# Performance work log

Measured on AMD Instinct MI355X. Metric: run time of the kernel, lower is better.

The kernel has to match this reference:

```python
import jax, jax.numpy as jnp
import numpy as np

N_NODES = 100000
NUM_ETYPE = 4
HEADS = 4
HID = 32
IN_CH = 128
EDGE_CH = 32
N_EDGES = 800000
BATCH = 1024
NEG = 5


def setup_inputs() -> dict:
    key = jax.random.key(0)
    ks = jax.random.split(key, 24)

    def w(k, shape, s=0.05):
        return jax.random.normal(k, shape, dtype=jnp.float32) * s

    inp = {}
    inp["edge_index"] = jax.random.randint(ks[0], (2, N_EDGES), 0, N_NODES)
    inp["edge_type"] = jax.random.randint(ks[1], (N_EDGES,), 0, NUM_ETYPE)
    inp["n_id"] = jax.random.randint(ks[2], (BATCH * (2 + NEG),), 0, N_NODES)
    inp["neg_sample_num"] = NEG
    inp["id_emb"] = w(ks[3], (N_NODES, IN_CH), 0.1)
    dims = [IN_CH, HEADS * HID]
    for i in range(2):
        d_in = dims[i]
        base = 4 + i * 7
        inp[f"W{i}"] = w(ks[base], (d_in, HEADS * HID))
        inp[f"Wres{i}"] = w(ks[base + 1], (d_in, HEADS * HID))
        inp[f"al{i}"] = w(ks[base + 2], (HEADS, HID))
        inp[f"ar{i}"] = w(ks[base + 3], (HEADS, HID))
        inp[f"ae{i}"] = w(ks[base + 4], (HEADS, EDGE_CH))
        inp[f"eemb{i}"] = w(ks[base + 5], (NUM_ETYPE, EDGE_CH))
        inp[f"We{i}"] = w(ks[base + 6], (EDGE_CH, HEADS * EDGE_CH))
    inp["pW1"] = w(ks[18], (2 * HEADS * HID, HID))
    inp["pb1"] = jnp.zeros((HID,), jnp.float32)
    inp["pW2"] = w(ks[19], (HID, 1))
    inp["pb2"] = jnp.zeros((1,), jnp.float32)
    return inp


def _leaky(x):
    return jnp.where(x > 0, x, 0.2 * x)  # LeakyReLU(0.2)


def _conv(h, src, dst, etype, W, Wres, al, ar, ae, eemb, We):
    """Simple-HGN style edge-typed graph attention conv with linear residual."""
    n = h.shape[0]
    feat = (h @ W).reshape(n, HEADS, HID)                      # [N,H,D]
    ef = (eemb @ We).reshape(NUM_ETYPE, HEADS, EDGE_CH)        # [T,H,De]
    el = jnp.einsum('nhd,hd->nh', feat, al)                    # [N,H]
    er = jnp.einsum('nhd,hd->nh', feat, ar)                    # [N,H]
    ee = jnp.einsum('thd,hd->th', ef, ae)                      # [T,H]
    logits = _leaky(el[src] + er[dst] + ee[etype])             # [E,H]
    # numerically stable per-destination softmax over incoming edges
    m = jax.ops.segment_max(logits, dst, num_segments=n)
    m = jnp.where(jnp.isfinite(m), m, jnp.zeros_like(m))
    a = jnp.exp(logits - m[dst])
    denom = jax.ops.segment_sum(a, dst, num_segments=n)
    alpha = a / (denom[dst] + 1e-16)                           # [E,H]
    out = jax.ops.segment_sum(feat[src] * alpha[:, :, None], dst, num_segments=n)
    return out.reshape(n, HEADS * HID) + h @ Wres


def reference(edge_index, edge_type, n_id, neg_sample_num, id_emb,
              W0, Wres0, al0, ar0, ae0, eemb0, We0,
              W1, Wres1, al1, ar1, ae1, eemb1, We1,
              pW1, pb1, pW2, pb2):
    src, dst = edge_index[0], edge_index[1]
    x = _conv(id_emb, src, dst, edge_type, W0, Wres0, al0, ar0, ae0, eemb0, We0)
    x = jax.nn.relu(x)  # relu between layers; dropout inactive at eval
    x = _conv(x, src, dst, edge_type, W1, Wres1, al1, ar1, ae1, eemb1, We1)
    b = n_id.shape[0] // (2 + neg_sample_num)
    out = x[n_id[:b]]
    pos = x[n_id[b:2 * b]]
    neg = x[n_id[2 * b:]]
    tiled = jnp.repeat(out, neg_sample_num, axis=0)  # repeat(1,neg).reshape(-1,D)

    def head(z):
        return _leaky(z @ pW1 + pb1) @ pW2 + pb2

    pos_logit = head(jnp.concatenate([out, pos], axis=-1))
    neg_logits = head(jnp.concatenate([tiled, neg], axis=-1))
    return pos_logit, neg_logits
```

## Files before the change

kernel.cpp:

```cpp
#include <hip/hip_runtime.h>
#include <hip/hip_bf16.h>
#include <math.h>

#define HEADS 4
#define HID 32
#define DIM 128
#define NEGS 5

typedef short s16x8 __attribute__((ext_vector_type(8)));
typedef short s16x4 __attribute__((ext_vector_type(4)));
typedef unsigned short u16x8 __attribute__((ext_vector_type(8)));
typedef float f32x4 __attribute__((ext_vector_type(4)));

__device__ __forceinline__ unsigned short f2bf_rn(float x) {
    unsigned int u = __float_as_uint(x);
    unsigned int r = (u + 0x7FFFu + ((u >> 16) & 1u)) >> 16;
    return (unsigned short)r;
}
__device__ __forceinline__ float bf2f(unsigned short b) {
    return __uint_as_float(((unsigned int)b) << 16);
}

__global__ void k_setup(const float* __restrict__ W0, const float* __restrict__ Wres0,
                        const float* __restrict__ W1, const float* __restrict__ Wres1,
                        const float* __restrict__ eemb0, const float* __restrict__ We0,
                        const float* __restrict__ ae0,
                        const float* __restrict__ eemb1, const float* __restrict__ We1,
                        const float* __restrict__ ae1,
                        unsigned short* __restrict__ bt, float* __restrict__ eeB,
                        int* __restrict__ zbase, int zn) {
    int idx = blockIdx.x * 256 + threadIdx.x;

    for (int i = idx; i < zn; i += 65536) zbase[i] = 0;

    {
        int layer = idx >> 15;
        int r = idx & 32767;
        int k = r >> 8;
        int n = r & 255;
        const float* src = layer ? ((n < 128) ? W1 : Wres1) : ((n < 128) ? W0 : Wres0);
        float x = src[k * 128 + (n & 127)];
        unsigned short h = f2bf_rn(x);
        unsigned short l = f2bf_rn(x - bf2f(h));
        unsigned short* base = bt + (size_t)layer * 2 * 32768;
        base[n * 128 + k] = h;
        base[32768 + n * 128 + k] = l;
    }

    if (idx < 32) {
        int layer = idx >> 4, t = idx & 15;
        const float* eemb = layer ? eemb1 : eemb0;
        const float* We   = layer ? We1 : We0;
        const float* ae   = layer ? ae1 : ae0;
        int et = t >> 2, h = t & 3;
        float s = 0.f;
        for (int d = 0; d < 32; ++d) {
            float ef = 0.f;
            for (int k = 0; k < 32; ++k) ef += eemb[et * 32 + k] * We[k * DIM + h * 32 + d];
            s += ef * ae[h * 32 + d];
        }
        eeB[layer * 16 + t] = s;
    }
}

__global__ void k_flag2(const int* __restrict__ n_id, int* __restrict__ flag2,
                        int* __restrict__ flag1, int M) {
    int i = blockIdx.x * 256 + threadIdx.x;
    if (i < M) { int n = n_id[i]; flag2[n] = 1; flag1[n] = 1; }
}

__global__ void k_histflag(const int* __restrict__ src, const int* __restrict__ dst,
                           const int* __restrict__ flag2,
                           int* __restrict__ counts, int* __restrict__ flag1, int E) {
    int e = blockIdx.x * 256 + threadIdx.x;
    if (e < E) {
        int d = dst[e];
        atomicAdd(&counts[d], 1);
        if (flag2[d]) flag1[src[e]] = 1;
    }
}

__global__ __launch_bounds__(1024) void k_scanA(const int* __restrict__ counts,
                                                int* __restrict__ rowtmp,
                                                int* __restrict__ bsum, int N) {
    __shared__ int s[1024];
    int i = blockIdx.x * 1024 + threadIdx.x;
    int v = (i < N) ? counts[i] : 0;
    s[threadIdx.x] = v;
    __syncthreads();
    for (int off = 1; off < 1024; off <<= 1) {
        int t = (threadIdx.x >= off) ? s[threadIdx.x - off] : 0;
        __syncthreads();
        s[threadIdx.x] += t;
        __syncthreads();
    }
    if (i < N) rowtmp[i] = s[threadIdx.x];
    if (threadIdx.x == 1023) bsum[blockIdx.x] = s[1023];
}

__global__ __launch_bounds__(256) void k_scanC(const int* __restrict__ rowtmp,
                                               const int* __restrict__ counts,
                                               const int* __restrict__ bsum, int nb,
                                               int* __restrict__ row_start,
                                               int* __restrict__ cursor,
                                               const int* __restrict__ flag1,
                                               const int* __restrict__ flag2,
                                               int* __restrict__ list1,
                                               int* __restrict__ list2,
                                               int* __restrict__ cnt1,
                                               int* __restrict__ cnt2, int N) {
    __shared__ int sex[128];
    int tid = threadIdx.x;
    if (tid < 64) {
        int l = tid;
        int a = (2 * l < nb) ? bsum[2 * l] : 0;
        int b = (2 * l + 1 < nb) ? bsum[2 * l + 1] : 0;
        int s = a + b;
        for (int off = 1; off < 64; off <<= 1) {
            int t = __shfl_up(s, off);
            if (l >= off) s += t;
        }
        int excl = s - (a + b);
        sex[2 * l] = excl;
        sex[2 * l + 1] = excl + a;
    }
    __syncthreads();

    int i = blockIdx.x * 256 + tid;
    int lane = tid & 63;
    if (i < N) {
        int st = rowtmp[i] - counts[i] + sex[i >> 10];
        row_start[i] = st;
        cursor[i] = st;
    }

    unsigned long long lt = (lane == 63) ? ~0ull >> 1 : (1ull << lane) - 1;
    bool a = (i < N) && flag1[i];
    unsigned long long m = __ballot(a);
    int base = 0;
    if (lane == 0 && m) base = atomicAdd(cnt1, __popcll(m));
    base = __shfl(base, 0);
    if (a) list1[base + __popcll(m & lt)] = i;

    bool b = (i < N) && flag2[i];
    m = __ballot(b);
    base = 0;
    if (lane == 0 && m) base = atomicAdd(cnt2, __popcll(m));
    base = __shfl(base, 0);
    if (b) list2[base + __popcll(m & lt)] = i;
}

__global__ void k_scatter(const int* __restrict__ dst, int* __restrict__ cursor,
                          int* __restrict__ csr_edge, int E) {
    int e = blockIdx.x * 256 + threadIdx.x;
    if (e < E) {
        int p = atomicAdd(&cursor[dst[e]], 1);
        csr_edge[p] = e;
    }
}

__global__ __launch_bounds__(256, 4) void k_gemm_fused(const float* __restrict__ A,
                                                       const unsigned short* __restrict__ Bhi,
                                                       const unsigned short* __restrict__ Blo,
                                                       unsigned short* __restrict__ featb,
                                                       float* __restrict__ res,
                                                       const float* __restrict__ al,
                                                       const float* __restrict__ ar,
                                                       float* __restrict__ el,
                                                       float* __restrict__ er,
                                                       const int* __restrict__ rowlist,
                                                       const int* __restrict__ rowcnt,
                                                       const int* __restrict__ resflag,
                                                       int N) {
    int limit = rowcnt ? *rowcnt : N;
    int c = blockIdx.x;
    int m0 = blockIdx.y * 64;
    if (m0 >= limit) return;

    __shared__ unsigned short Bh[8192];
    __shared__ unsigned short Bl[8192];
    int tid = threadIdx.x;
    int lane = tid & 63, w = tid >> 6;
    int wm = (w & 1) * 32, wn = (w >> 1) * 32;
    int lr = lane & 15, g = lane >> 4;

#pragma unroll
    for (int i = 0; i < 4; ++i) {
        int f = tid + i * 256;
        int row = f >> 4, g16 = f & 15;
        int off = (row * 256 + ((g16 * 16) ^ ((row & 7) << 4))) >> 1;
        *(u16x8*)&Bh[off] = *(const u16x8*)(Bhi + (size_t)(c * 64 + row) * DIM + g16 * 8);
        *(u16x8*)&Bl[off] = *(const u16x8*)(Blo + (size_t)(c * 64 + row) * DIM + g16 * 8);
    }

    s16x8 afh[2][4], afl[2][4];
#pragma unroll
    for (int fm = 0; fm < 2; ++fm) {
        int idx = m0 + wm + fm * 16 + lr;
        bool valid = idx < limit;
        int grow = 0;
        if (valid) grow = rowlist ? rowlist[idx] : idx;
        const float* ap = A + (size_t)grow * DIM;
#pragma unroll
        for (int ks = 0; ks < 4; ++ks) {
            float4 p = make_float4(0.f, 0.f, 0.f, 0.f);
            float4 q = make_float4(0.f, 0.f, 0.f, 0.f);
            if (valid) {
                p = *(const float4*)(ap + ks * 32 + g * 4);
                q = *(const float4*)(ap + ks * 32 + 16 + g * 4);
            }
            float vv[8] = {p.x, p.y, p.z, p.w, q.x, q.y, q.z, q.w};
            s16x8 hv, lv;
#pragma unroll
            for (int j = 0; j < 8; ++j) {
                unsigned short hh = f2bf_rn(vv[j]);
                hv[j] = (short)hh;
                lv[j] = (short)f2bf_rn(vv[j] - bf2f(hh));
            }
            afh[fm][ks] = hv;
            afl[fm][ks] = lv;
        }
    }
    __syncthreads();

    f32x4 acc[2][2];
#pragma unroll
    for (int fm = 0; fm < 2; ++fm)
#pragma unroll
        for (int fn = 0; fn < 2; ++fn) acc[fm][fn] = (f32x4){0.f, 0.f, 0.f, 0.f};

#pragma unroll
    for (int ks = 0; ks < 4; ++ks) {
        s16x8 bfh[2], bfl[2];
#pragma unroll
        for (int fn = 0; fn < 2; ++fn) {
            int row = wn + fn * 16 + lr;
            int sw = (row & 7) << 4;
            int o1 = (row * 256 + ((ks * 64 + g * 8) ^ sw)) >> 1;
            int o2 = (row * 256 + ((ks * 64 + 32 + g * 8) ^ sw)) >> 1;
            s16x4 p = *(const s16x4*)&Bh[o1];
            s16x4 q = *(const s16x4*)&Bh[o2];
            bfh[fn] = (s16x8){p[0], p[1], p[2], p[3], q[0], q[1], q[2], q[3]};
            p = *(const s16x4*)&Bl[o1];
            q = *(const s16x4*)&Bl[o2];
            bfl[fn] = (s16x8){p[0], p[1], p[2], p[3], q[0], q[1], q[2], q[3]};
        }
#pragma unroll
        for (int fm = 0; fm < 2; ++fm)
#pragma unroll
            for (int fn = 0; fn < 2; ++fn) {
                acc[fm][fn] = __builtin_amdgcn_mfma_f32_16x16x32_bf16(afh[fm][ks], bfh[fn], acc[fm][fn], 0, 0, 0);
                acc[fm][fn] = __builtin_amdgcn_mfma_f32_16x16x32_bf16(afh[fm][ks], bfl[fn], acc[fm][fn], 0, 0, 0);
                acc[fm][fn] = __builtin_amdgcn_mfma_f32_16x16x32_bf16(afl[fm][ks], bfh[fn], acc[fm][fn], 0, 0, 0);
            }
    }

#pragma unroll
    for (int fm = 0; fm < 2; ++fm)
#pragma unroll
        for (int fn = 0; fn < 2; ++fn) {
            int idx0 = m0 + wm + fm * 16 + g * 4;
            int dc = ((c * 64) & 127) + wn + fn * 16 + lr;
#pragma unroll
            for (int r = 0; r < 4; ++r) {
                int idx = idx0 + r;
                if (idx < limit) {
                    int gr = rowlist ? rowlist[idx] : idx;
                    if (c < 2) {
                        featb[(size_t)gr * DIM + dc] = f2bf_rn(acc[fm][fn][r]);
                    } else if (!resflag || resflag[gr]) {
                        res[(size_t)gr * DIM + dc] = acc[fm][fn][r];
                    }
                }
            }
        }

    if (c < 2) {
        int h = c * 2 + (wn >> 5);
        float a0 = al[h * HID + lr], a1 = al[h * HID + 16 + lr];
        float b0 = ar[h * HID + lr], b1 = ar[h * HID + 16 + lr];
#pragma unroll
        for (int fm = 0; fm < 2; ++fm)
#pragma unroll
            for (int r = 0; r < 4; ++r) {
                float ev = acc[fm][0][r] * a0 + acc[fm][1][r] * a1;
                float rv = acc[fm][0][r] * b0 + acc[fm][1][r] * b1;
#pragma unroll
                for (int off = 1; off < 16; off <<= 1) {
                    ev += __shfl_xor(ev, off);
                    rv += __shfl_xor(rv, off);
                }
                if (lr == 0) {
                    int idx = m0 + wm + fm * 16 + g * 4 + r;
                    if (idx < limit) {
                        int node = rowlist ? rowlist[idx] : idx;
                        el[node * 4 + h] = ev;
                        er[node * 4 + h] = rv;
                    }
                }
            }
    }
}

template <int RELU>
__global__ __launch_bounds__(256) void k_agg(const unsigned short* __restrict__ featb,
                                             const float* __restrict__ el,
                                             const float* __restrict__ er,
                                             const float* __restrict__ eeB,
                                             const int* __restrict__ srcArr,
                                             const int* __restrict__ etArr,
                                             const int* __restrict__ csr_edge,
                                             const int* __restrict__ row_start,
                                             const int* __restrict__ counts,
                                             const int* __restrict__ dlist,
                                             const int* __restrict__ dcnt,
                                             float* __restrict__ out) {
    int wv = threadIdx.x >> 6;
    int lane = threadIdx.x & 63;
    int idx = blockIdx.x * 4 + wv;
    if (idx >= *dcnt) return;
    int node = dlist[idx];

    int beg = row_start[node];
    int deg = counts[node];
    int eh = lane & 3;
    float er_v = er[node * 4 + eh];

    float m = -INFINITY;
    for (int base = 0; base < deg; base += 16) {
        int ei = base + (lane >> 2);
        float lg = -INFINITY;
        if (ei < deg) {
            int e = csr_edge[beg + ei];
            float x = el[srcArr[e] * 4 + eh] + er_v + eeB[etArr[e] * 4 + eh];
            lg = (x > 0.f) ? x : 0.2f * x;
        }
        m = fmaxf(m, lg);
    }
    for (int off = 4; off < 64; off <<= 1) m = fmaxf(m, __shfl_xor(m, off));

    float denom = 0.f, acc0 = 0.f, acc1 = 0.f;
    int h1 = lane >> 5;
    for (int base = 0; base < deg; base += 16) {
        int ei = base + (lane >> 2);
        float wgt = 0.f;
        int s = 0;
        if (ei < deg) {
            int e = csr_edge[beg + ei];
            s = srcArr[e];
            float x = el[s * 4 + eh] + er_v + eeB[etArr[e] * 4 + eh];
            x = (x > 0.f) ? x : 0.2f * x;
            wgt = expf(x - m);
            denom += wgt;
        }
        int cnt = min(16, deg - base);
        for (int j = 0; j < cnt; ++j) {
            int sj = __shfl(s, j * 4);
            float w1 = __shfl(wgt, j * 4 + h1);
            float w2 = __shfl(wgt, j * 4 + 2 + h1);
            acc0 += w1 * bf2f(featb[(size_t)sj * DIM + lane]);
            acc1 += w2 * bf2f(featb[(size_t)sj * DIM + 64 + lane]);
        }
    }
    for (int off = 4; off < 64; off <<= 1) denom += __shfl_xor(denom, off);
    float d1 = __shfl(denom, h1);
    float d2 = __shfl(denom, 2 + h1);

    float r0 = out[(size_t)node * DIM + lane] + acc0 / (d1 + 1e-16f);
    float r1 = out[(size_t)node * DIM + 64 + lane] + acc1 / (d2 + 1e-16f);
    if (RELU) { r0 = fmaxf(r0, 0.f); r1 = fmaxf(r1, 0.f); }
    out[(size_t)node * DIM + lane] = r0;
    out[(size_t)node * DIM + 64 + lane] = r1;
}

__global__ __launch_bounds__(256) void k_head(const float* __restrict__ x1,
                                              const int* __restrict__ n_id,
                                              const float* __restrict__ pW1,
                                              const float* __restrict__ pb1,
                                              const float* __restrict__ pW2,
                                              const float* __restrict__ pb2,
                                              float* __restrict__ dout, int B) {
    int o = blockIdx.x * 4 + (threadIdx.x >> 6);
    int lane = threadIdx.x & 63;
    int total = B + B * NEGS;
    if (o >= total) return;
    int a, c;
    if (o < B) { a = n_id[o]; c = n_id[B + o]; }
    else { int j = o - B; a = n_id[j / NEGS]; c = n_id[2 * B + j]; }

    int j = lane & 31;
    int half = lane >> 5;
    int row = half ? c : a;
    const float* z = x1 + (size_t)row * DIM;
    const float* w = pW1 + (half ? 128 * 32 : 0);
    float t = 0.f;
#pragma unroll 8
    for (int k = 0; k < 128; ++k) t += z[k] * w[k * 32 + j];
    t += __shfl_xor(t, 32);
    t += pb1[j];
    t = (t > 0.f) ? t : 0.2f * t;
    float r = t * pW2[j];
    for (int off = 1; off < 32; off <<= 1) r += __shfl_xor(r, off);
    if (lane == 0) dout[o] = r + pb2[0];
}

extern "C" void kernel_launch(void* const* d_in, const int* in_sizes, int n_in,
                              void* d_out, int out_size, void* d_ws, size_t ws_size,
                              hipStream_t stream) {
    const int* edge_index = (const int*)d_in[0];
    const int* etype      = (const int*)d_in[1];
    const int* n_id       = (const int*)d_in[2];
    const float* id_emb   = (const float*)d_in[4];
    const float* W0    = (const float*)d_in[5];
    const float* Wres0 = (const float*)d_in[6];
    const float* al0   = (const float*)d_in[7];
    const float* ar0   = (const float*)d_in[8];
    const float* ae0   = (const float*)d_in[9];
    const float* eemb0 = (const float*)d_in[10];
    const float* We0   = (const float*)d_in[11];
    const float* W1    = (const float*)d_in[12];
    const float* Wres1 = (const float*)d_in[13];
    const float* al1   = (const float*)d_in[14];
    const float* ar1   = (const float*)d_in[15];
    const float* ae1   = (const float*)d_in[16];
    const float* eemb1 = (const float*)d_in[17];
    const float* We1   = (const float*)d_in[18];
    const float* pW1   = (const float*)d_in[19];
    const float* pb1   = (const float*)d_in[20];
    const float* pW2   = (const float*)d_in[21];
    const float* pb2   = (const float*)d_in[22];

    int E = in_sizes[1];
    int N = in_sizes[4] / DIM;
    int M = in_sizes[2];
    int B = M / (2 + NEGS);
    const int* srcArr = edge_index;
    const int* dstArr = edge_index + E;

    size_t N128 = (size_t)N * DIM;
    unsigned short* featb = (unsigned short*)d_ws;
    float* x0   = (float*)(featb + N128);
    float* x1   = x0 + N128;
    float* el   = x1 + N128;
    float* er   = el + (size_t)N * 4;
    float* eeB  = er + (size_t)N * 4;
    int* counts    = (int*)(eeB + 32);
    int* flag1     = counts + N;
    int* flag2     = flag1 + N;
    int* cnt1      = flag2 + N;
    int* cnt2      = cnt1 + 1;
    int* rowtmp    = cnt2 + 1;
    int* row_start = rowtmp + N;
    int* cursor    = row_start + N;
    int* csr_edge  = cursor + N;
    int* list1     = csr_edge + E;
    int* list2     = list1 + N;
    int* bsum      = list2 + M;
    unsigned short* bt = (unsigned short*)(bsum + 256);

    k_setup<<<256, 256, 0, stream>>>(W0, Wres0, W1, Wres1,
                                     eemb0, We0, ae0, eemb1, We1, ae1,
                                     bt, eeB, counts, 3 * N + 2);

    k_flag2<<<(M + 255) / 256, 256, 0, stream>>>(n_id, flag2, flag1, M);
    k_histflag<<<(E + 255) / 256, 256, 0, stream>>>(srcArr, dstArr, flag2, counts, flag1, E);
    int nb = (N + 1023) / 1024;
    k_scanA<<<nb, 1024, 0, stream>>>(counts, rowtmp, bsum, N);
    k_scanC<<<(N + 255) / 256, 256, 0, stream>>>(rowtmp, counts, bsum, nb, row_start, cursor,
                                                 flag1, flag2, list1, list2, cnt1, cnt2, N);
    k_scatter<<<(E + 255) / 256, 256, 0, stream>>>(dstArr, cursor, csr_edge, E);

    dim3 ggrid(4, (N + 63) / 64);
    int aggGridFull = (N + 3) / 4;
    int aggGridS2 = (M + 3) / 4;

    k_gemm_fused<<<ggrid, 256, 0, stream>>>(id_emb, bt, bt + 32768, featb, x0,
                                            al0, ar0, el, er, nullptr, nullptr, flag1, N);
    k_agg<1><<<aggGridFull, 256, 0, stream>>>(featb, el, er, eeB, srcArr, etype, csr_edge,
                                              row_start, counts, list1, cnt1, x0);

    k_gemm_fused<<<ggrid, 256, 0, stream>>>(x0, bt + 65536, bt + 98304, featb, x1,
                                            al1, ar1, el, er, list1, cnt1, flag2, N);
    k_agg<0><<<aggGridS2, 256, 0, stream>>>(featb, el, er, eeB + 16, srcArr, etype, csr_edge,
                                            row_start, counts, list2, cnt2, x1);

    int total = B * (1 + NEGS);
    k_head<<<(total + 3) / 4, 256, 0, stream>>>(x1, n_id, pW1, pb1, pW2, pb2,
                                                (float*)d_out, B);
}
```

Baseline: 369.6 us.

## Retile GEMM warps to 16x64 and vectorize bf16 gathers in aggregation

The GEMM kernel now gives each warp 16 rows by all 64 columns, where before it covered a 32x32 tile. Each warp converts one A row-fragment, and all four B fragments are read from shared memory per k-step, which changes the LDS traffic and register profile. The aggregation kernel now has each lane load two adjacent bf16 features with one 32-bit gather instead of two 16-bit loads. It also uses a single head weight per lane and float2 reads and writes of the output. The goal is fewer memory instructions in the edge gather loop, which dominates the runtime.

After: 338.4 us, median of 2. -8.4%, faster.

```diff
diff --git a/kernel.cpp b/kernel.cpp
--- a/kernel.cpp
+++ b/kernel.cpp
@@ -181,7 +181,6 @@
     __shared__ unsigned short Bl[8192];
     int tid = threadIdx.x;
     int lane = tid & 63, w = tid >> 6;
-    int wm = (w & 1) * 32, wn = (w >> 1) * 32;
     int lr = lane & 15, g = lane >> 4;
 
 #pragma unroll
@@ -193,13 +192,12 @@
         *(u16x8*)&Bl[off] = *(const u16x8*)(Blo + (size_t)(c * 64 + row) * DIM + g16 * 8);
     }
 
-    s16x8 afh[2][4], afl[2][4];
-#pragma unroll
-    for (int fm = 0; fm < 2; ++fm) {
-        int idx = m0 + wm + fm * 16 + lr;
-        bool valid = idx < limit;
+    s16x8 afh[4], afl[4];
+    {
+        int aidx = m0 + w * 16 + lr;
+        bool valid = aidx < limit;
         int grow = 0;
-        if (valid) grow = rowlist ? rowlist[idx] : idx;
+        if (valid) grow = rowlist ? rowlist[aidx] : aidx;
         const float* ap = A + (size_t)grow * DIM;
 #pragma unroll
         for (int ks = 0; ks < 4; ++ks) {
@@ -217,24 +215,22 @@
                 hv[j] = (short)hh;
                 lv[j] = (short)f2bf_rn(vv[j] - bf2f(hh));
             }
-            afh[fm][ks] = hv;
-            afl[fm][ks] = lv;
+            afh[ks] = hv;
+            afl[ks] = lv;
         }
     }
     __syncthreads();
 
-    f32x4 acc[2][2];
-#pragma unroll
-    for (int fm = 0; fm < 2; ++fm)
-#pragma unroll
-        for (int fn = 0; fn < 2; ++fn) acc[fm][fn] = (f32x4){0.f, 0.f, 0.f, 0.f};
+    f32x4 acc[4];
+#pragma unroll
+    for (int fn = 0; fn < 4; ++fn) acc[fn] = (f32x4){0.f, 0.f, 0.f, 0.f};
 
 #pragma unroll
     for (int ks = 0; ks < 4; ++ks) {
-        s16x8 bfh[2], bfl[2];
-#pragma unroll
-        for (int fn = 0; fn < 2; ++fn) {
-            int row = wn + fn * 16 + lr;
+        s16x8 bfh[4], bfl[4];
+#pragma unroll
+        for (int fn = 0; fn < 4; ++fn) {
+            int row = fn * 16 + lr;
             int sw = (row & 7) << 4;
             int o1 = (row * 256 + ((ks * 64 + g * 8) ^ sw)) >> 1;
             int o2 = (row * 256 + ((ks * 64 + 32 + g * 8) ^ sw)) >> 1;
@@ -246,59 +242,61 @@
             bfl[fn] = (s16x8){p[0], p[1], p[2], p[3], q[0], q[1], q[2], q[3]};
         }
 #pragma unroll
-        for (int fm = 0; fm < 2; ++fm)
-#pragma unroll
-            for (int fn = 0; fn < 2; ++fn) {
-                acc[fm][fn] = __builtin_amdgcn_mfma_f32_16x16x32_bf16(afh[fm][ks], bfh[fn], acc[fm][fn], 0, 0, 0);
-                acc[fm][fn] = __builtin_amdgcn_mfma_f32_16x16x32_bf16(afh[fm][ks], bfl[fn], acc[fm][fn], 0, 0, 0);
-                acc[fm][fn] = __builtin_amdgcn_mfma_f32_16x16x32_bf16(afl[fm][ks], bfh[fn], acc[fm][fn], 0, 0, 0);
+        for (int fn = 0; fn < 4; ++fn) {
+            acc[fn] = __builtin_amdgcn_mfma_f32_16x16x32_bf16(afh[ks], bfh[fn], acc[fn], 0, 0, 0);
+            acc[fn] = __builtin_amdgcn_mfma_f32_16x16x32_bf16(afh[ks], bfl[fn], acc[fn], 0, 0, 0);
+            acc[fn] = __builtin_amdgcn_mfma_f32_16x16x32_bf16(afl[ks], bfh[fn], acc[fn], 0, 0, 0);
+        }
+    }
+
+    int idx0 = m0 + w * 16 + g * 4;
+#pragma unroll
+    for (int fn = 0; fn < 4; ++fn) {
+        int dc = ((c * 64) & 127) + fn * 16 + lr;
+#pragma unroll
+        for (int r = 0; r < 4; ++r) {
+            int idx = idx0 + r;
+            if (idx < limit) {
+                int gr = rowlist ? rowlist[idx] : idx;
+                if (c < 2) {
+                    featb[(size_t)gr * DIM + dc] = f2bf_rn(acc[fn][r]);
+                } else if (!resflag || resflag[gr]) {
+                    res[(size_t)gr * DIM + dc] = acc[fn][r];
+                }
             }
-    }
-
-#pragma unroll
-    for (int fm = 0; fm < 2; ++fm)
-#pragma unroll
-        for (int fn = 0; fn < 2; ++fn) {
-            int idx0 = m0 + wm + fm * 16 + g * 4;
-            int dc = ((c * 64) & 127) + wn + fn * 16 + lr;
-#pragma unroll
-            for (int r = 0; r < 4; ++r) {
+        }
+    }
+
+    if (c < 2) {
+        int h0 = c * 2, h1 = c * 2 + 1;
+        float a00 = al[h0 * HID + lr], a01 = al[h0 * HID + 16 + lr];
+        float a10 = al[h1 * HID + lr], a11 = al[h1 * HID + 16 + lr];
+        float b00 = ar[h0 * HID + lr], b01 = ar[h0 * HID + 16 + lr];
+        float b10 = ar[h1 * HID + lr], b11 = ar[h1 * HID + 16 + lr];
+#pragma unroll
+        for (int r = 0; r < 4; ++r) {
+            float ev0 = acc[0][r] * a00 + acc[1][r] * a01;
+            float rv0 = acc[0][r] * b00 + acc[1][r] * b01;
+            float ev1 = acc[2][r] * a10 + acc[3][r] * a11;
+            float rv1 = acc[2][r] * b10 + acc[3][r] * b11;
+#pragma unroll
+            for (int off = 1; off < 16; off <<= 1) {
+                ev0 += __shfl_xor(ev0, off);
+                rv0 += __shfl_xor(rv0, off);
+                ev1 += __shfl_xor(ev1, off);
+                rv1 += __shfl_xor(rv1, off);
+            }
+            if (lr == 0) {
                 int idx = idx0 + r;
                 if (idx < limit) {
-                    int gr = rowlist ? rowlist[idx] : idx;
-                    if (c < 2) {
-                        featb[(size_t)gr * DIM + dc] = f2bf_rn(acc[fm][fn][r]);
-                    } else if (!resflag || resflag[gr]) {
-                        res[(size_t)gr * DIM + dc] = acc[fm][fn][r];
-                    }
+                    int node = rowlist ? rowlist[idx] : idx;
+                    el[node * 4 + h0] = ev0;
+                    er[node * 4 + h0] = rv0;
+                    el[node * 4 + h1] = ev1;
+                    er[node * 4 + h1] = rv1;
                 }
             }
         }
-
-    if (c < 2) {
-        int h = c * 2 + (wn >> 5);
-        float a0 = al[h * HID + lr], a1 = al[h * HID + 16 + lr];
-        float b0 = ar[h * HID + lr], b1 = ar[h * HID + 16 + lr];
-#pragma unroll
-        for (int fm = 0; fm < 2; ++fm)
-#pragma unroll
-            for (int r = 0; r < 4; ++r) {
-                float ev = acc[fm][0][r] * a0 + acc[fm][1][r] * a1;
-                float rv = acc[fm][0][r] * b0 + acc[fm][1][r] * b1;
-#pragma unroll
-                for (int off = 1; off < 16; off <<= 1) {
-                    ev += __shfl_xor(ev, off);
-                    rv += __shfl_xor(rv, off);
-                }
-                if (lr == 0) {
-                    int idx = m0 + wm + fm * 16 + g * 4 + r;
-                    if (idx < limit) {
-                        int node = rowlist ? rowlist[idx] : idx;
-                        el[node * 4 + h] = ev;
-                        er[node * 4 + h] = rv;
-                    }
-                }
-            }
     }
 }
 
@@ -324,6 +322,7 @@
     int beg = row_start[node];
     int deg = counts[node];
     int eh = lane & 3;
+    int hc = lane >> 4;
     float er_v = er[node * 4 + eh];
 
     float m = -INFINITY;
@@ -340,7 +339,6 @@
     for (int off = 4; off < 64; off <<= 1) m = fmaxf(m, __shfl_xor(m, off));
 
     float denom = 0.f, acc0 = 0.f, acc1 = 0.f;
-    int h1 = lane >> 5;
     for (int base = 0; base < deg; base += 16) {
         int ei = base + (lane >> 2);
         float wgt = 0.f;
@@ -356,21 +354,20 @@
         int cnt = min(16, deg - base);
         for (int j = 0; j < cnt; ++j) {
             int sj = __shfl(s, j * 4);
-            float w1 = __shfl(wgt, j * 4 + h1);
-            float w2 = __shfl(wgt, j * 4 + 2 + h1);
-            acc0 += w1 * bf2f(featb[(size_t)sj * DIM + lane]);
-            acc1 += w2 * bf2f(featb[(size_t)sj * DIM + 64 + lane]);
+            float ww = __shfl(wgt, j * 4 + hc);
+            unsigned int pv = *(const unsigned int*)(featb + (size_t)sj * DIM + 2 * lane);
+            acc0 += ww * bf2f((unsigned short)(pv & 0xFFFFu));
+            acc1 += ww * bf2f((unsigned short)(pv >> 16));
         }
     }
     for (int off = 4; off < 64; off <<= 1) denom += __shfl_xor(denom, off);
-    float d1 = __shfl(denom, h1);
-    float d2 = __shfl(denom, 2 + h1);
-
-    float r0 = out[(size_t)node * DIM + lane] + acc0 / (d1 + 1e-16f);
-    float r1 = out[(size_t)node * DIM + 64 + lane] + acc1 / (d2 + 1e-16f);
+    float d = __shfl(denom, hc);
+
+    float2 prev = *(const float2*)(out + (size_t)node * DIM + 2 * lane);
+    float r0 = prev.x + acc0 / (d + 1e-16f);
+    float r1 = prev.y + acc1 / (d + 1e-16f);
     if (RELU) { r0 = fmaxf(r0, 0.f); r1 = fmaxf(r1, 0.f); }
-    out[(size_t)node * DIM + lane] = r0;
-    out[(size_t)node * DIM + 64 + lane] = r1;
+    *(float2*)(out + (size_t)node * DIM + 2 * lane) = make_float2(r0, r1);
 }
 
 __global__ __launch_bounds__(256) void k_head(const float* __restrict__ x1,
```
